# Kernel tuning notes

Measured on AMD Instinct MI355X. Metric: run time of the kernel, lower is better.

Reference implementation:

```python
import jax, jax.numpy as jnp
import numpy as np

SIGMA = (2.0, 5.0, 10.0, 20.0, 40.0, 60.0)  # RBF bandwidths from __init__
MAX_SEG = 16  # static upper bound on number of class segments (== n classes in gt)


def setup_inputs() -> dict:
    key = jax.random.key(0)
    k1, k2, k3 = jax.random.split(key, 3)
    B, C, H, W = 1, 128, 64, 64
    predict = jax.random.normal(k1, (B, C, H, W), dtype=jnp.float32)
    target = jax.random.normal(k2, (B, C, H, W), dtype=jnp.float32)
    # sorted_randint -> contiguous variable-size class segments, as the torch loop assumes
    gt = jnp.sort(jax.random.randint(k3, (B * H * W,), 0, MAX_SEG)).reshape(B, H, W)
    ignore_mask = jnp.ones((B, H, W), dtype=bool)  # all pixels visible
    return {"predict": predict, "target": target, "gt": gt, "ignore_mask": ignore_mask}


def _sqdist(a, b):
    # ||a_i - b_j||^2 ; prob_mat in the original is -0.5 * this
    aa = jnp.sum(a * a, axis=1)
    bb = jnp.sum(b * b, axis=1)
    return aa[:, None] + bb[None, :] - 2.0 * (a @ b.T)


def reference(predict, target, gt, ignore_mask):
    d = predict.shape[1]
    # [B,C,H,W] -> [V,C]; ignore_mask is all True so visible set == all pixels
    pf = predict.transpose(0, 2, 3, 1).reshape(-1, d)
    tf = target.transpose(0, 2, 3, 1).reshape(-1, d)
    cls = gt.reshape(-1)

    # segment id = index of contiguous class run (what the Python boundary loop computes)
    boundary = (cls[1:] != cls[:-1]).astype(jnp.int32)
    seg = jnp.concatenate([jnp.zeros((1,), jnp.int32), jnp.cumsum(boundary)])
    counts = jax.ops.segment_sum(jnp.ones(seg.shape, predict.dtype), seg, num_segments=MAX_SEG)

    # pairwise squared distances within/between predict and target (shared across segments)
    Dpp = _sqdist(pf, pf)
    Dtt = _sqdist(tf, tf)
    Dpt = _sqdist(pf, tf)

    # Per segment with M=N=n: ww is +1/(2n^2) on pp/tt blocks, -1/(2n^2) on cross blocks,
    # and sum over the tp block equals sum over the pt block. So
    # loss_s = (1/(2 n^2)) * sum_bw sum_{i,j in s} (Kpp + Ktt - 2 Kpt)_{ij}
    C = jnp.zeros_like(Dpp)
    for bw in SIGMA:
        inv = -0.5 / bw  # K = exp(prob/bw) = exp(-||x_i-x_j||^2 / (2 bw))
        C = C + jnp.exp(inv * Dpp) + jnp.exp(inv * Dtt) - 2.0 * jnp.exp(inv * Dpt)

    same = seg[:, None] == seg[None, :]
    C = jnp.where(same, C, 0.0)
    seg_tot = jax.ops.segment_sum(jnp.sum(C, axis=1), seg, num_segments=MAX_SEG)

    denom = jnp.maximum(2.0 * counts * counts, 1.0)
    loss_s = jnp.where(counts > 0, seg_tot / denom, 0.0)
    pos = loss_s > 0
    loss_s = jnp.where(pos, jnp.sqrt(jnp.where(pos, loss_s, 1.0)), 0.0)  # sqrt(loss) if >0 else 0

    class_count = jnp.sum(counts > 0).astype(predict.dtype)
    return jnp.sum(loss_s) / class_count
```

## Files before the change

kernel.cpp:

```cpp
#include <hip/hip_runtime.h>
#include <math.h>

#define NCLS 16
#define TS   64
#define CH   32
#define ROWK 40
#define NB   256
#define PIXB 16

typedef float vfloat4 __attribute__((ext_vector_type(4), aligned(4)));
typedef short bf16x8 __attribute__((ext_vector_type(8)));
typedef float f32x4  __attribute__((ext_vector_type(4)));

struct Ctl {
    int   counts[NCLS];
    int   starts[NCLS + 1];
    int   tpc[NCLS];
    int   pairBase[NCLS + 1];
    float classSum[NCLS];
};

__device__ __forceinline__ unsigned bf16_hi(float x) {
    unsigned u = __float_as_uint(x);
    return (u + 0x7FFFu + ((u >> 16) & 1u)) >> 16;
}
__device__ __forceinline__ float bf16_f(unsigned h) {
    return __uint_as_float(h << 16);
}

__global__ __launch_bounds__(256) void prep_kernel(
    const float* __restrict__ P, const float* __restrict__ T,
    const int* __restrict__ gt, int V, int D,
    Ctl* __restrict__ ctl,
    float* __restrict__ normP, float* __restrict__ normT,
    int nbNorm) {
    const int b = blockIdx.x;
    const int t = threadIdx.x;
    if (b < nbNorm) {
        __shared__ float pP[16][PIXB + 1], pT[16][PIXB + 1];
        const int pix = t & (PIXB - 1);
        const int dl  = t >> 4;
        const int v   = b * PIXB + pix;
        float np = 0.f, nt = 0.f;
        if (v < V) {
            #pragma unroll 4
            for (int d = dl; d < D; d += 16) {
                float x = P[(long)d * V + v]; np += x * x;
                float y = T[(long)d * V + v]; nt += y * y;
            }
        }
        pP[dl][pix] = np; pT[dl][pix] = nt;
        __syncthreads();
        if (t < PIXB && b * PIXB + t < V) {
            float sp = 0.f, st = 0.f;
            #pragma unroll
            for (int k = 0; k < 16; ++k) { sp += pP[k][t]; st += pT[k][t]; }
            normP[b * PIXB + t] = sp;
            normT[b * PIXB + t] = st;
        }
    } else {
        if (t < NCLS) {
            int lo = 0, hi = V;
            while (lo < hi) {
                int mid = (lo + hi) >> 1;
                if (gt[mid] < t) lo = mid + 1; else hi = mid;
            }
            ctl->starts[t] = lo;
            ctl->classSum[t] = 0.0f;
        }
        if (t == 0) ctl->starts[NCLS] = V;
        __syncthreads();
        if (t == 0) {
            int pb = 0;
            for (int c = 0; c < NCLS; ++c) {
                int n = ctl->starts[c + 1] - ctl->starts[c];
                ctl->counts[c] = n;
                int tp = (n + TS - 1) / TS;
                ctl->tpc[c] = tp;
                ctl->pairBase[c] = pb;
                pb += tp * (tp + 1) / 2;
            }
            ctl->pairBase[NCLS] = pb;
        }
    }
}

__global__ __launch_bounds__(256) void mmd_kernel(
    const float* __restrict__ P, const float* __restrict__ T,
    int V, int D, const Ctl* __restrict__ ctl,
    const float* __restrict__ normP, const float* __restrict__ normT,
    float* __restrict__ classSum)
{
    __shared__ unsigned short sRhP[TS][ROWK], sRlP[TS][ROWK];
    __shared__ unsigned short sRhT[TS][ROWK], sRlT[TS][ROWK];
    __shared__ unsigned short sChP[TS][ROWK], sClP[TS][ROWK];
    __shared__ unsigned short sChT[TS][ROWK], sClT[TS][ROWK];
    __shared__ float wsum[4];

    const int t    = threadIdx.x;
    const int lane = t & 63;
    const int wv   = t >> 6;
    const int half = t >> 7;
    const int sdp  = (t >> 3) & 15;
    const int qb   = t & 7;

    const int W = ctl->pairBase[NCLS];
    const float invs[6] = {-0.25f, -0.1f, -0.05f, -0.025f, -0.0125f, -1.0f/120.0f};

    for (int w = blockIdx.x; w < W; w += gridDim.x) {
        int c = 0;
        while (ctl->pairBase[c + 1] <= w) ++c;
        const int tp = ctl->tpc[c];
        int rem = w - ctl->pairBase[c];
        int ti = 0;
        while (rem >= tp - ti) { rem -= (tp - ti); ++ti; }
        const int tj    = ti + rem;
        const bool diag = (ti == tj);
        const int n     = ctl->counts[c];
        const int start = ctl->starts[c];
        const int i0    = ti * TS;
        const int j0    = tj * TS;

        const int qbase = (half ? j0 : i0) + 4 * qb;

        auto load_quad = [&](long off, int rb, vfloat4& vP, vfloat4& vT) {
            if (rb + 3 < n) {
                vP = *(const vfloat4*)&P[off + start + rb];
                vT = *(const vfloat4*)&T[off + start + rb];
            } else {
                int a0 = start + min(rb,     n - 1);
                int a1 = start + min(rb + 1, n - 1);
                int a2 = start + min(rb + 2, n - 1);
                int a3 = start + min(rb + 3, n - 1);
                vP = (vfloat4){P[off + a0], P[off + a1], P[off + a2], P[off + a3]};
                vT = (vfloat4){T[off + a0], T[off + a1], T[off + a2], T[off + a3]};
            }
        };

        vfloat4 vP0a, vP0b, vT0a, vT0b, vP1a, vP1b, vT1a, vT1b;
        auto issue_loads = [&](int dcc) {
            if (half && diag) return;
            const long o0 = (long)(dcc + 2 * sdp)     * (long)V;
            const long o1 = (long)(dcc + 2 * sdp + 1) * (long)V;
            load_quad(o0, qbase,      vP0a, vT0a);
            load_quad(o0, qbase + 32, vP0b, vT0b);
            load_quad(o1, qbase,      vP1a, vT1a);
            load_quad(o1, qbase + 32, vP1b, vT1b);
        };

        const unsigned short (*pBhP)[ROWK] = diag ? sRhP : sChP;
        const unsigned short (*pBlP)[ROWK] = diag ? sRlP : sClP;
        const unsigned short (*pBhT)[ROWK] = diag ? sRhT : sChT;
        const unsigned short (*pBlT)[ROWK] = diag ? sRlT : sClT;

        f32x4 aPP[4], aPT[4], aTT[4], aTP[4];
        #pragma unroll
        for (int cs = 0; cs < 4; ++cs) {
            aPP[cs] = (f32x4){0.f,0.f,0.f,0.f};
            aPT[cs] = (f32x4){0.f,0.f,0.f,0.f};
            aTT[cs] = (f32x4){0.f,0.f,0.f,0.f};
            aTP[cs] = (f32x4){0.f,0.f,0.f,0.f};
        }

        issue_loads(0);

        #pragma unroll 1
        for (int dc = 0; dc < D; dc += CH) {
            __syncthreads();
            if (!(half && diag)) {
                unsigned short (*dHP)[ROWK] = half ? sChP : sRhP;
                unsigned short (*dLP)[ROWK] = half ? sClP : sRlP;
                unsigned short (*dHT)[ROWK] = half ? sChT : sRhT;
                unsigned short (*dLT)[ROWK] = half ? sClT : sRlT;
                #pragma unroll
                for (int g = 0; g < 2; ++g) {
                    const vfloat4 p0 = g ? vP0b : vP0a, p1 = g ? vP1b : vP1a;
                    const vfloat4 t0 = g ? vT0b : vT0a, t1 = g ? vT1b : vT1a;
                    #pragma unroll
                    for (int i = 0; i < 4; ++i) {
                        const int px = 4 * qb + 32 * g + i;
                        unsigned h0, h1, l0, l1;
                        h0 = bf16_hi(p0[i]); l0 = bf16_hi(p0[i] - bf16_f(h0));
                        h1 = bf16_hi(p1[i]); l1 = bf16_hi(p1[i] - bf16_f(h1));
                        *(unsigned*)&dHP[px][2*sdp] = h0 | (h1 << 16);
                        *(unsigned*)&dLP[px][2*sdp] = l0 | (l1 << 16);
                        h0 = bf16_hi(t0[i]); l0 = bf16_hi(t0[i] - bf16_f(h0));
                        h1 = bf16_hi(t1[i]); l1 = bf16_hi(t1[i] - bf16_f(h1));
                        *(unsigned*)&dHT[px][2*sdp] = h0 | (h1 << 16);
                        *(unsigned*)&dLT[px][2*sdp] = l0 | (l1 << 16);
                    }
                }
            }
            __syncthreads();
            if (dc + CH < D)
                issue_loads(dc + CH);

            const int am = 16 * wv + (lane & 15);
            const int ko = (lane >> 4) * 8;
            bf16x8 aPh = *(const bf16x8*)&sRhP[am][ko];
            bf16x8 aPl = *(const bf16x8*)&sRlP[am][ko];
            bf16x8 aTh = *(const bf16x8*)&sRhT[am][ko];
            bf16x8 aTl = *(const bf16x8*)&sRlT[am][ko];
            #pragma unroll 1
            for (int cs = 0; cs < 4; ++cs) {
                const int bn = 16 * cs + (lane & 15);
                bf16x8 bPh = *(const bf16x8*)&pBhP[bn][ko];
                bf16x8 bPl = *(const bf16x8*)&pBlP[bn][ko];
                bf16x8 bTh = *(const bf16x8*)&pBhT[bn][ko];
                bf16x8 bTl = *(const bf16x8*)&pBlT[bn][ko];
                aPP[cs] = __builtin_amdgcn_mfma_f32_16x16x32_bf16(aPh, bPh, aPP[cs], 0,0,0);
                aPP[cs] = __builtin_amdgcn_mfma_f32_16x16x32_bf16(aPh, bPl, aPP[cs], 0,0,0);
                aPP[cs] = __builtin_amdgcn_mfma_f32_16x16x32_bf16(aPl, bPh, aPP[cs], 0,0,0);
                aPT[cs] = __builtin_amdgcn_mfma_f32_16x16x32_bf16(aPh, bTh, aPT[cs], 0,0,0);
                aPT[cs] = __builtin_amdgcn_mfma_f32_16x16x32_bf16(aPh, bTl, aPT[cs], 0,0,0);
                aPT[cs] = __builtin_amdgcn_mfma_f32_16x16x32_bf16(aPl, bTh, aPT[cs], 0,0,0);
                aTT[cs] = __builtin_amdgcn_mfma_f32_16x16x32_bf16(aTh, bTh, aTT[cs], 0,0,0);
                aTT[cs] = __builtin_amdgcn_mfma_f32_16x16x32_bf16(aTh, bTl, aTT[cs], 0,0,0);
                aTT[cs] = __builtin_amdgcn_mfma_f32_16x16x32_bf16(aTl, bTh, aTT[cs], 0,0,0);
                aTP[cs] = __builtin_amdgcn_mfma_f32_16x16x32_bf16(aTh, bPh, aTP[cs], 0,0,0);
                aTP[cs] = __builtin_amdgcn_mfma_f32_16x16x32_bf16(aTh, bPl, aTP[cs], 0,0,0);
                aTP[cs] = __builtin_amdgcn_mfma_f32_16x16x32_bf16(aTl, bPh, aTP[cs], 0,0,0);
            }
        }

        const float f = diag ? 1.0f : 2.0f;
        float total = 0.0f;
        float nPi[4], nTi[4];
        #pragma unroll
        for (int r = 0; r < 4; ++r) {
            const int iiL = 16 * wv + (lane >> 4) * 4 + r;
            const int gi  = start + min(i0 + iiL, n - 1);
            nPi[r] = normP[gi];
            nTi[r] = normT[gi];
        }
        #pragma unroll
        for (int cs = 0; cs < 4; ++cs) {
            const int jj = j0 + 16 * cs + (lane & 15);
            if (jj < n) {
                const float nPj = normP[start + jj];
                const float nTj = normT[start + jj];
                #pragma unroll
                for (int r = 0; r < 4; ++r) {
                    const int ii = i0 + 16 * wv + (lane >> 4) * 4 + r;
                    if (ii < n) {
                        float Dpp = nPi[r] + nPj - 2.0f * aPP[cs][r];
                        float Dtt = nTi[r] + nTj - 2.0f * aTT[cs][r];
                        float Dpt = nPi[r] + nTj - 2.0f * aPT[cs][r];
                        float Dtp = nTi[r] + nPj - 2.0f * aTP[cs][r];
                        float s6 = 0.0f;
                        #pragma unroll
                        for (int s = 0; s < 6; ++s) {
                            s6 += __expf(invs[s] * Dpp) + __expf(invs[s] * Dtt)
                                - __expf(invs[s] * Dpt) - __expf(invs[s] * Dtp);
                        }
                        total += f * s6;
                    }
                }
            }
        }

        #pragma unroll
        for (int off = 32; off > 0; off >>= 1)
            total += __shfl_down(total, off, 64);
        if (lane == 0) wsum[wv] = total;
        __syncthreads();
        if (t == 0)
            atomicAdd(&classSum[c], wsum[0] + wsum[1] + wsum[2] + wsum[3]);
    }
}

__global__ void finalize_kernel(const int* __restrict__ counts,
                                const float* __restrict__ classSum,
                                float* __restrict__ out) {
    if (threadIdx.x == 0) {
        float loss = 0.0f;
        int k = 0;
        for (int c = 0; c < NCLS; ++c) {
            int n = counts[c];
            if (n > 0) {
                ++k;
                float fn    = (float)n;
                float denom = fmaxf(2.0f * fn * fn, 1.0f);
                float l     = classSum[c] / denom;
                if (l > 0.0f) loss += sqrtf(l);
            }
        }
        out[0] = (k > 0) ? (loss / (float)k) : 0.0f;
    }
}

extern "C" void kernel_launch(void* const* d_in, const int* in_sizes, int n_in,
                              void* d_out, int out_size, void* d_ws, size_t ws_size,
                              hipStream_t stream) {
    const float* predict = (const float*)d_in[0];
    const float* target  = (const float*)d_in[1];
    const int*   gt      = (const int*)d_in[2];

    const int V = in_sizes[2];
    const int D = in_sizes[0] / V;

    Ctl* ctl = (Ctl*)d_ws;
    size_t normOff = (sizeof(Ctl) + 15) & ~(size_t)15;
    float* normP = (float*)((char*)d_ws + normOff);
    float* normT = normP + V;
    float* classSum = (float*)((char*)d_ws + offsetof(Ctl, classSum));

    int nbNorm = (V + PIXB - 1) / PIXB;
    prep_kernel<<<nbNorm + 1, 256, 0, stream>>>(predict, target, gt, V, D,
                                                ctl, normP, normT, nbNorm);

    mmd_kernel<<<NB, 256, 0, stream>>>(predict, target, V, D, ctl,
                                       normP, normT, classSum);

    finalize_kernel<<<1, 64, 0, stream>>>(ctl->counts, classSum, (float*)d_out);
}
```

Measured before the change: 89.17 us.

## Precompute bf16 hi/lo split in pixel-major layout during prep kernel

The prep kernel gains 128 extra blocks that convert predict and target once into bf16 high/low pairs, transposed to a pixel-major [V][D] layout in workspace. The MMD kernel then loads contiguous 16-byte bf16 chunks per pixel straight into LDS, with no per-tile split-conversion or strided channel-major gathers. This removes repeated conversion work and uncoalesced loads across tile pairs, at the cost of an extra global write/read pass of 4 bf16 arrays. The transpose indexing hard-codes 64 blocks per tensor (V*D/8/4 threads), so it assumes V=4096, D=128.

```diff
diff --git a/kernel.cpp b/kernel.cpp
--- a/kernel.cpp
+++ b/kernel.cpp
@@ -11,6 +11,7 @@
 typedef float vfloat4 __attribute__((ext_vector_type(4), aligned(4)));
 typedef short bf16x8 __attribute__((ext_vector_type(8)));
 typedef float f32x4  __attribute__((ext_vector_type(4)));
+typedef unsigned short u16x8 __attribute__((ext_vector_type(8)));
 
 struct Ctl {
     int   counts[NCLS];
@@ -33,6 +34,8 @@
     const int* __restrict__ gt, int V, int D,
     Ctl* __restrict__ ctl,
     float* __restrict__ normP, float* __restrict__ normT,
+    unsigned short* __restrict__ XhP, unsigned short* __restrict__ XlP,
+    unsigned short* __restrict__ XhT, unsigned short* __restrict__ XlT,
     int nbNorm) {
     const int b = blockIdx.x;
     const int t = threadIdx.x;
@@ -58,7 +61,7 @@
             normP[b * PIXB + t] = sp;
             normT[b * PIXB + t] = st;
         }
-    } else {
+    } else if (b == nbNorm) {
         if (t < NCLS) {
             int lo = 0, hi = V;
             while (lo < hi) {
@@ -82,27 +85,53 @@
             }
             ctl->pairBase[NCLS] = pb;
         }
+    } else {
+        const int idx = b - nbNorm - 1;
+        const bool isT = idx >= 64;
+        const float* S = isT ? T : P;
+        unsigned short* Xh = isT ? XhT : XhP;
+        unsigned short* Xl = isT ? XlT : XlP;
+        const int u   = (idx & 63) * 256 + t;
+        const int v0  = (u & 1023) * 4;
+        const int d0  = (u >> 10) * 8;
+        vfloat4 val[8];
+        #pragma unroll
+        for (int k = 0; k < 8; ++k)
+            val[k] = *(const vfloat4*)&S[(long)(d0 + k) * V + v0];
+        #pragma unroll
+        for (int i = 0; i < 4; ++i) {
+            u16x8 h, l;
+            #pragma unroll
+            for (int k = 0; k < 8; ++k) {
+                unsigned hh = bf16_hi(val[k][i]);
+                h[k] = (unsigned short)hh;
+                l[k] = (unsigned short)bf16_hi(val[k][i] - bf16_f(hh));
+            }
+            *(u16x8*)&Xh[(long)(v0 + i) * D + d0] = h;
+            *(u16x8*)&Xl[(long)(v0 + i) * D + d0] = l;
+        }
     }
 }
 
 __global__ __launch_bounds__(256) void mmd_kernel(
-    const float* __restrict__ P, const float* __restrict__ T,
+    const unsigned short* __restrict__ XhP, const unsigned short* __restrict__ XlP,
+    const unsigned short* __restrict__ XhT, const unsigned short* __restrict__ XlT,
     int V, int D, const Ctl* __restrict__ ctl,
     const float* __restrict__ normP, const float* __restrict__ normT,
     float* __restrict__ classSum)
 {
-    __shared__ unsigned short sRhP[TS][ROWK], sRlP[TS][ROWK];
-    __shared__ unsigned short sRhT[TS][ROWK], sRlT[TS][ROWK];
-    __shared__ unsigned short sChP[TS][ROWK], sClP[TS][ROWK];
-    __shared__ unsigned short sChT[TS][ROWK], sClT[TS][ROWK];
+    __shared__ unsigned short sR[4][TS][ROWK];
+    __shared__ unsigned short sC[4][TS][ROWK];
     __shared__ float wsum[4];
 
     const int t    = threadIdx.x;
     const int lane = t & 63;
     const int wv   = t >> 6;
-    const int half = t >> 7;
-    const int sdp  = (t >> 3) & 15;
-    const int qb   = t & 7;
+    const int spx  = t & 63;
+    const int sar  = t >> 6;
+
+    const unsigned short* Xa = (sar == 0) ? XhP : (sar == 1) ? XlP
+                             : (sar == 2) ? XhT : XlT;
 
     const int W = ctl->pairBase[NCLS];
     const float invs[6] = {-0.25f, -0.1f, -0.05f, -0.025f, -0.0125f, -1.0f/120.0f};
@@ -121,37 +150,27 @@
         const int i0    = ti * TS;
         const int j0    = tj * TS;
 
-        const int qbase = (half ? j0 : i0) + 4 * qb;
-
-        auto load_quad = [&](long off, int rb, vfloat4& vP, vfloat4& vT) {
-            if (rb + 3 < n) {
-                vP = *(const vfloat4*)&P[off + start + rb];
-                vT = *(const vfloat4*)&T[off + start + rb];
-            } else {
-                int a0 = start + min(rb,     n - 1);
-                int a1 = start + min(rb + 1, n - 1);
-                int a2 = start + min(rb + 2, n - 1);
-                int a3 = start + min(rb + 3, n - 1);
-                vP = (vfloat4){P[off + a0], P[off + a1], P[off + a2], P[off + a3]};
-                vT = (vfloat4){T[off + a0], T[off + a1], T[off + a2], T[off + a3]};
+        const long gr = (long)(start + min(i0 + spx, n - 1)) * D;
+        const long gc = (long)(start + min(j0 + spx, n - 1)) * D;
+
+        uint4 r0, r1, r2, r3, c0, c1, c2, c3;
+        auto issue_loads = [&](int dcc) {
+            const unsigned short* pr = Xa + gr + dcc;
+            r0 = *(const uint4*)(pr);
+            r1 = *(const uint4*)(pr + 8);
+            r2 = *(const uint4*)(pr + 16);
+            r3 = *(const uint4*)(pr + 24);
+            if (!diag) {
+                const unsigned short* pc = Xa + gc + dcc;
+                c0 = *(const uint4*)(pc);
+                c1 = *(const uint4*)(pc + 8);
+                c2 = *(const uint4*)(pc + 16);
+                c3 = *(const uint4*)(pc + 24);
             }
         };
 
-        vfloat4 vP0a, vP0b, vT0a, vT0b, vP1a, vP1b, vT1a, vT1b;
-        auto issue_loads = [&](int dcc) {
-            if (half && diag) return;
-            const long o0 = (long)(dcc + 2 * sdp)     * (long)V;
-            const long o1 = (long)(dcc + 2 * sdp + 1) * (long)V;
-            load_quad(o0, qbase,      vP0a, vT0a);
-            load_quad(o0, qbase + 32, vP0b, vT0b);
-            load_quad(o1, qbase,      vP1a, vT1a);
-            load_quad(o1, qbase + 32, vP1b, vT1b);
-        };
-
-        const unsigned short (*pBhP)[ROWK] = diag ? sRhP : sChP;
-        const unsigned short (*pBlP)[ROWK] = diag ? sRlP : sClP;
-        const unsigned short (*pBhT)[ROWK] = diag ? sRhT : sChT;
-        const unsigned short (*pBlT)[ROWK] = diag ? sRlT : sClT;
+        typedef unsigned short lds_arr[TS][ROWK];
+        const lds_arr* pB = diag ? sR : sC;
 
         f32x4 aPP[4], aPT[4], aTT[4], aTP[4];
         #pragma unroll
@@ -167,29 +186,15 @@
         #pragma unroll 1
         for (int dc = 0; dc < D; dc += CH) {
             __syncthreads();
-            if (!(half && diag)) {
-                unsigned short (*dHP)[ROWK] = half ? sChP : sRhP;
-                unsigned short (*dLP)[ROWK] = half ? sClP : sRlP;
-                unsigned short (*dHT)[ROWK] = half ? sChT : sRhT;
-                unsigned short (*dLT)[ROWK] = half ? sClT : sRlT;
-                #pragma unroll
-                for (int g = 0; g < 2; ++g) {
-                    const vfloat4 p0 = g ? vP0b : vP0a, p1 = g ? vP1b : vP1a;
-                    const vfloat4 t0 = g ? vT0b : vT0a, t1 = g ? vT1b : vT1a;
-                    #pragma unroll
-                    for (int i = 0; i < 4; ++i) {
-                        const int px = 4 * qb + 32 * g + i;
-                        unsigned h0, h1, l0, l1;
-                        h0 = bf16_hi(p0[i]); l0 = bf16_hi(p0[i] - bf16_f(h0));
-                        h1 = bf16_hi(p1[i]); l1 = bf16_hi(p1[i] - bf16_f(h1));
-                        *(unsigned*)&dHP[px][2*sdp] = h0 | (h1 << 16);
-                        *(unsigned*)&dLP[px][2*sdp] = l0 | (l1 << 16);
-                        h0 = bf16_hi(t0[i]); l0 = bf16_hi(t0[i] - bf16_f(h0));
-                        h1 = bf16_hi(t1[i]); l1 = bf16_hi(t1[i] - bf16_f(h1));
-                        *(unsigned*)&dHT[px][2*sdp] = h0 | (h1 << 16);
-                        *(unsigned*)&dLT[px][2*sdp] = l0 | (l1 << 16);
-                    }
-                }
+            *(uint4*)&sR[sar][spx][0]  = r0;
+            *(uint4*)&sR[sar][spx][8]  = r1;
+            *(uint4*)&sR[sar][spx][16] = r2;
+            *(uint4*)&sR[sar][spx][24] = r3;
+            if (!diag) {
+                *(uint4*)&sC[sar][spx][0]  = c0;
+                *(uint4*)&sC[sar][spx][8]  = c1;
+                *(uint4*)&sC[sar][spx][16] = c2;
+                *(uint4*)&sC[sar][spx][24] = c3;
             }
             __syncthreads();
             if (dc + CH < D)
@@ -197,17 +202,17 @@
 
             const int am = 16 * wv + (lane & 15);
             const int ko = (lane >> 4) * 8;
-            bf16x8 aPh = *(const bf16x8*)&sRhP[am][ko];
-            bf16x8 aPl = *(const bf16x8*)&sRlP[am][ko];
-            bf16x8 aTh = *(const bf16x8*)&sRhT[am][ko];
-            bf16x8 aTl = *(const bf16x8*)&sRlT[am][ko];
+            bf16x8 aPh = *(const bf16x8*)&sR[0][am][ko];
+            bf16x8 aPl = *(const bf16x8*)&sR[1][am][ko];
+            bf16x8 aTh = *(const bf16x8*)&sR[2][am][ko];
+            bf16x8 aTl = *(const bf16x8*)&sR[3][am][ko];
             #pragma unroll 1
             for (int cs = 0; cs < 4; ++cs) {
                 const int bn = 16 * cs + (lane & 15);
-                bf16x8 bPh = *(const bf16x8*)&pBhP[bn][ko];
-                bf16x8 bPl = *(const bf16x8*)&pBlP[bn][ko];
-                bf16x8 bTh = *(const bf16x8*)&pBhT[bn][ko];
-                bf16x8 bTl = *(const bf16x8*)&pBlT[bn][ko];
+                bf16x8 bPh = *(const bf16x8*)&pB[0][bn][ko];
+                bf16x8 bPl = *(const bf16x8*)&pB[1][bn][ko];
+                bf16x8 bTh = *(const bf16x8*)&pB[2][bn][ko];
+                bf16x8 bTl = *(const bf16x8*)&pB[3][bn][ko];
                 aPP[cs] = __builtin_amdgcn_mfma_f32_16x16x32_bf16(aPh, bPh, aPP[cs], 0,0,0);
                 aPP[cs] = __builtin_amdgcn_mfma_f32_16x16x32_bf16(aPh, bPl, aPP[cs], 0,0,0);
                 aPP[cs] = __builtin_amdgcn_mfma_f32_16x16x32_bf16(aPl, bPh, aPP[cs], 0,0,0);
@@ -299,17 +304,24 @@
     const int V = in_sizes[2];
     const int D = in_sizes[0] / V;
 
-    Ctl* ctl = (Ctl*)d_ws;
-    size_t normOff = (sizeof(Ctl) + 15) & ~(size_t)15;
-    float* normP = (float*)((char*)d_ws + normOff);
-    float* normT = normP + V;
+    char* ws = (char*)d_ws;
+    Ctl* ctl = (Ctl*)ws;
+    size_t off = (sizeof(Ctl) + 255) & ~(size_t)255;
+    float* normP = (float*)(ws + off);                 off += (size_t)V * 4;
+    float* normT = (float*)(ws + off);                 off += (size_t)V * 4;
+    off = (off + 255) & ~(size_t)255;
+    unsigned short* XhP = (unsigned short*)(ws + off); off += (size_t)V * D * 2;
+    unsigned short* XlP = (unsigned short*)(ws + off); off += (size_t)V * D * 2;
+    unsigned short* XhT = (unsigned short*)(ws + off); off += (size_t)V * D * 2;
+    unsigned short* XlT = (unsigned short*)(ws + off);
     float* classSum = (float*)((char*)d_ws + offsetof(Ctl, classSum));
 
     int nbNorm = (V + PIXB - 1) / PIXB;
-    prep_kernel<<<nbNorm + 1, 256, 0, stream>>>(predict, target, gt, V, D,
-                                                ctl, normP, normT, nbNorm);
-
-    mmd_kernel<<<NB, 256, 0, stream>>>(predict, target, V, D, ctl,
+    prep_kernel<<<nbNorm + 1 + 128, 256, 0, stream>>>(
+        predict, target, gt, V, D, ctl, normP, normT,
+        XhP, XlP, XhT, XlT, nbNorm);
+
+    mmd_kernel<<<NB, 256, 0, stream>>>(XhP, XlP, XhT, XlT, V, D, ctl,
                                        normP, normT, classSum);
 
     finalize_kernel<<<1, 64, 0, stream>>>(ctl->counts, classSum, (float*)d_out);
```

New measurement: 87.75 us. About the same (-1.6%).
